# Optimization experiments

Hardware: AMD Instinct MI355X
Metric: run time of the kernel (lower is better)

Reference implementation:

```python
import jax, jax.numpy as jnp
import numpy as np
from itertools import product

DIM = 384
HEADS = 8
DIM_HEAD = 64
INNER = HEADS * DIM_HEAD  # 512
KS = 3                    # kernel_size (attention window)
PAD = KS // 2
W_WIN = KS * KS           # 9
SCALE = DIM_HEAD ** -0.5


def setup_inputs() -> dict:
    key = jax.random.key(0)
    k1, k2, k3, k4, k5 = jax.random.split(key, 5)
    B, H, W = 4, 56, 56
    x = jax.random.normal(k1, (B, DIM, H, W), dtype=jnp.float32)
    # 1x1 conv weights stored as (out_ch, in_ch)
    Wq = jax.random.normal(k2, (INNER, DIM), dtype=jnp.float32) * (DIM ** -0.5)
    Wkv = jax.random.normal(k3, (2 * INNER, DIM), dtype=jnp.float32) * (DIM ** -0.5)
    Wo = jax.random.normal(k4, (DIM, INNER), dtype=jnp.float32) * (INNER ** -0.5)
    bo = jax.random.normal(k5, (DIM,), dtype=jnp.float32) * 0.01
    return {"x": x, "Wq": Wq, "Wkv": Wkv, "Wo": Wo, "bo": bo}


def _conv1x1(x, w):
    # x: (B,Cin,H,W), w: (Cout,Cin) -> (B,Cout,H,W)
    return jnp.einsum('bchw,oc->bohw', x, w)


def reference(x, Wq, Wkv, Wo, bo):
    B, C, H, W = x.shape
    q = _conv1x1(x, Wq)                       # (B, INNER, H, W)
    kv = _conv1x1(x, Wkv)                     # (B, 2*INNER, H, W)
    k, v = jnp.split(kv, 2, axis=1)
    # split channels heads-major, matching torch reshape (B, heads, dh, H, W)
    q = q.reshape(B, HEADS, DIM_HEAD, H, W)
    k = k.reshape(B, HEADS, DIM_HEAD, H, W)
    v = v.reshape(B, HEADS, DIM_HEAD, H, W)
    # zero-pad spatial dims (matches F.unfold zero padding: padded taps get logit 0)
    k_pad = jnp.pad(k, ((0, 0), (0, 0), (0, 0), (PAD, PAD), (PAD, PAD)))
    v_pad = jnp.pad(v, ((0, 0), (0, 0), (0, 0), (PAD, PAD), (PAD, PAD)))
    offsets = list(product(range(KS), range(KS)))  # row-major = unfold order
    # dots: (B, heads, H, W, w)
    dots = jnp.stack([
        jnp.einsum('bhdxy,bhdxy->bhxy', q, k_pad[:, :, :, i:i + H, j:j + W])
        for (i, j) in offsets
    ], axis=-1) * SCALE
    attn = jax.nn.softmax(dots, axis=-1)      # softmax over the 9-tap window
    # weighted sum of shifted v: (B, heads, dh, H, W)
    out = sum(
        attn[:, :, None, :, :, w_idx] * v_pad[:, :, :, i:i + H, j:j + W]
        for w_idx, (i, j) in enumerate(offsets)
    )
    out = out.reshape(B, INNER, H, W)
    return _conv1x1(out, Wo) + bo[None, :, None, None]
```

## Files before the change

### kernel.cpp

```cpp
#include <hip/hip_runtime.h>


#define HW 3136
#define WIMG 56
#define QKV_CH 1536
#define SCALE 0.125f
#define SLEN 200

typedef __bf16 bf16x8_t __attribute__((ext_vector_type(8)));
typedef float f32x4_t __attribute__((ext_vector_type(4)));

__device__ __forceinline__ float bf2f(unsigned short u) {
    return __uint_as_float(((unsigned int)u) << 16);
}
__device__ __forceinline__ unsigned short f2bf(float f) {
    unsigned int u = __float_as_uint(f);
    u += 0x7FFFu + ((u >> 16) & 1u);
    return (unsigned short)(u >> 16);
}

__global__ __launch_bounds__(256) void cvt_w(
    const float* __restrict__ Wq, const float* __restrict__ Wkv,
    const float* __restrict__ Wo,
    unsigned short* __restrict__ wT, unsigned short* __restrict__ wT3)
{
    const int i = blockIdx.x * 256 + threadIdx.x;
    if (i < 73728) {
        const int g = i & 3;
        const int idx3 = i >> 2;
        const int o128 = idx3 & 127;
        const int rest = idx3 >> 7;
        const int kb = rest % 12, oblk = rest / 12;
        const int o = oblk * 128 + o128;
        const int k0 = kb * 32 + g * 8;
        const float* src = (o < 512) ? (Wq + (size_t)o * 384 + k0)
                                     : (Wkv + (size_t)(o - 512) * 384 + k0);
        const float4 v0 = *reinterpret_cast<const float4*>(src);
        const float4 v1 = *reinterpret_cast<const float4*>(src + 4);
        uint4 u;
        u.x = (unsigned int)f2bf(v0.x) | ((unsigned int)f2bf(v0.y) << 16);
        u.y = (unsigned int)f2bf(v0.z) | ((unsigned int)f2bf(v0.w) << 16);
        u.z = (unsigned int)f2bf(v1.x) | ((unsigned int)f2bf(v1.y) << 16);
        u.w = (unsigned int)f2bf(v1.z) | ((unsigned int)f2bf(v1.w) << 16);
        reinterpret_cast<uint4*>(wT)[i] = u;
    } else {
        const int j = i - 73728;
        const int g = j & 3;
        const int idx3 = j >> 2;
        const int o128 = idx3 & 127;
        const int rest = idx3 >> 7;
        const int kb = rest % 16, oblk = rest / 16;
        const int o = oblk * 128 + o128;
        const float* src = Wo + (size_t)o * 512 + kb * 32 + g * 8;
        const float4 v0 = *reinterpret_cast<const float4*>(src);
        const float4 v1 = *reinterpret_cast<const float4*>(src + 4);
        uint4 u;
        u.x = (unsigned int)f2bf(v0.x) | ((unsigned int)f2bf(v0.y) << 16);
        u.y = (unsigned int)f2bf(v0.z) | ((unsigned int)f2bf(v0.w) << 16);
        u.z = (unsigned int)f2bf(v1.x) | ((unsigned int)f2bf(v1.y) << 16);
        u.w = (unsigned int)f2bf(v1.z) | ((unsigned int)f2bf(v1.w) << 16);
        reinterpret_cast<uint4*>(wT3)[j] = u;
    }
}

__global__ __launch_bounds__(256) void cvtT_x(
    const float* __restrict__ x, unsigned short* __restrict__ xT)
{
    __shared__ unsigned short Tl[64 * 36];
    const int sblk = blockIdx.x, kblk = blockIdx.y, b = blockIdx.z;
    const int t = threadIdx.x;

    if (sblk == 49) {
        unsigned short* dst = xT + (((size_t)b * 25 + 24) * 12 + kblk) * 4096 + 2048;
        *reinterpret_cast<uint4*>(dst + t * 8) = (uint4){0, 0, 0, 0};
        return;
    }

    const float* xp = x + ((size_t)b * 384 + (size_t)kblk * 32) * HW + sblk * 64;
    const int c = t >> 3;
#pragma unroll
    for (int i = 0; i < 2; i++) {
        const int sc = (t & 7) + 8 * i;
        const float4 v = *reinterpret_cast<const float4*>(xp + (size_t)c * HW + sc * 4);
        const int s4 = sc * 4;
        Tl[(s4 + 0) * 36 + c] = f2bf(v.x);
        Tl[(s4 + 1) * 36 + c] = f2bf(v.y);
        Tl[(s4 + 2) * 36 + c] = f2bf(v.z);
        Tl[(s4 + 3) * 36 + c] = f2bf(v.w);
    }
    __syncthreads();

    const int row = t >> 2, gran = t & 3;
    const uint2 lo = *reinterpret_cast<const uint2*>(&Tl[row * 36 + gran * 8]);
    const uint2 hi = *reinterpret_cast<const uint2*>(&Tl[row * 36 + gran * 8 + 4]);
    uint4 o; o.x = lo.x; o.y = lo.y; o.z = hi.x; o.w = hi.y;
    unsigned short* dst = xT + (((size_t)b * 25 + (sblk >> 1)) * 12 + kblk) * 4096
                        + (sblk & 1) * 2048;
    *reinterpret_cast<uint4*>(dst + t * 8) = o;
}

__global__ __launch_bounds__(256) void gemm1(
    const unsigned short* __restrict__ xT,
    const unsigned short* __restrict__ wT,
    unsigned short* __restrict__ qkv)
{
    __shared__ __align__(16) unsigned short A_lds[128 * 32];
    __shared__ __align__(16) unsigned short B_lds[128 * 32];

    const int sblk = blockIdx.x;
    const int oblk = blockIdx.y;
    const int b  = blockIdx.z;
    const int t  = threadIdx.x;
    const int lane = t & 63, w = t >> 6;
    const int quad = lane >> 4, mrow = lane & 15;
    const int wm = w >> 1, wn = w & 1;

    const unsigned short* wsrc = wT + ((size_t)oblk * 12) * 4096;
    const unsigned short* xsrc = xT + (((size_t)b * 25 + sblk) * 12) * 4096;

    f32x4_t acc[4][4];
#pragma unroll
    for (int m = 0; m < 4; m++)
#pragma unroll
        for (int n = 0; n < 4; n++) acc[m][n] = (f32x4_t){0.f, 0.f, 0.f, 0.f};

    for (int kb = 0; kb < 12; kb++) {
        const uint4 a0 = *reinterpret_cast<const uint4*>(wsrc + (size_t)kb * 4096 + t * 8);
        const uint4 a1 = *reinterpret_cast<const uint4*>(wsrc + (size_t)kb * 4096 + 2048 + t * 8);
        const uint4 b0 = *reinterpret_cast<const uint4*>(xsrc + (size_t)kb * 4096 + t * 8);
        const uint4 b1 = *reinterpret_cast<const uint4*>(xsrc + (size_t)kb * 4096 + 2048 + t * 8);

        __syncthreads();
        *reinterpret_cast<uint4*>(A_lds + t * 8) = a0;
        *reinterpret_cast<uint4*>(A_lds + 2048 + t * 8) = a1;
        *reinterpret_cast<uint4*>(B_lds + t * 8) = b0;
        *reinterpret_cast<uint4*>(B_lds + 2048 + t * 8) = b1;
        __syncthreads();

        bf16x8_t af[4], bf[4];
#pragma unroll
        for (int m = 0; m < 4; m++)
            af[m] = *reinterpret_cast<const bf16x8_t*>(&A_lds[(wm * 64 + m * 16 + mrow) * 32 + quad * 8]);
#pragma unroll
        for (int n = 0; n < 4; n++)
            bf[n] = *reinterpret_cast<const bf16x8_t*>(&B_lds[(wn * 64 + n * 16 + mrow) * 32 + quad * 8]);
#pragma unroll
        for (int m = 0; m < 4; m++)
#pragma unroll
            for (int n = 0; n < 4; n++)
                acc[m][n] = __builtin_amdgcn_mfma_f32_16x16x32_bf16(af[m], bf[n], acc[m][n], 0, 0, 0);
    }

    const int o0 = oblk * 128 + wm * 64;
    const int s0 = sblk * 128 + wn * 64;
    unsigned short* outb = qkv + (size_t)b * QKV_CH * HW;
#pragma unroll
    for (int m = 0; m < 4; m++)
#pragma unroll
        for (int n = 0; n < 4; n++) {
            const int ss = s0 + n * 16 + mrow;
            if (ss < HW) {
#pragma unroll
                for (int r = 0; r < 4; r++) {
                    const int oo = o0 + m * 16 + quad * 4 + r;
                    outb[(size_t)oo * HW + ss] = f2bf(acc[m][n][r]);
                }
            }
        }
}

__global__ __launch_bounds__(256) void natt2(
    const unsigned short* __restrict__ qkv,
    unsigned short* __restrict__ aoT)
{
    __shared__ __align__(16) unsigned short smem[2 * 64 * SLEN];
    unsigned short* Kl = smem;
    unsigned short* Vl = smem + 64 * SLEN;
    float* dred = reinterpret_cast<float*>(smem);

    const int t = threadIdx.x, lane = t & 63, w = t >> 6;
    const int sblk = blockIdx.x;
    const int s0 = sblk * 64;
    const int s  = s0 + lane;
    const int h  = blockIdx.y, b = blockIdx.z;
    const int y  = s / WIMG, xx = s % WIMG;

    const size_t hbase = (size_t)b * QKV_CH * HW + (size_t)(h * 64) * HW;
    const unsigned short* kg = qkv + hbase + (size_t)512 * HW;
    const unsigned short* vg = qkv + hbase + (size_t)1024 * HW;

#pragma unroll
    for (int i = 0; i < 6; i++) {
        const int f = i * 256 + t;
        const int d = f / 24, j = f % 24;
        int g = s0 - 64 + j * 8;
        g = min(max(g, 0), HW - 8);
        const uint4 k4 = *reinterpret_cast<const uint4*>(kg + (size_t)d * HW + g);
        const uint4 v4 = *reinterpret_cast<const uint4*>(vg + (size_t)d * HW + g);
        *reinterpret_cast<uint4*>(&Kl[d * SLEN + j * 8]) = k4;
        *reinterpret_cast<uint4*>(&Vl[d * SLEN + j * 8]) = v4;
    }

    int   off9[9];
    float msk[9];
#pragma unroll
    for (int ty = 0; ty < 3; ty++)
#pragma unroll
        for (int tx = 0; tx < 3; tx++) {
            const int tap = ty * 3 + tx;
            const int ny = y + ty - 1, nx = xx + tx - 1;
            const bool v = (ny >= 0) && (ny < WIMG) && (nx >= 0) && (nx < WIMG);
            off9[tap] = v ? ((ty - 1) * WIMG + (tx - 1)) : 0;
            msk[tap]  = v ? 1.f : 0.f;
        }

    __syncthreads();

    const unsigned short* qp = qkv + hbase + s;
    float dots[9];
#pragma unroll
    for (int tp = 0; tp < 9; tp++) dots[tp] = 0.f;
#pragma unroll 4
    for (int dd = 0; dd < 16; dd++) {
        const int d = w * 16 + dd;
        const float qv = bf2f(qp[(size_t)d * HW]);
        const int bi = d * SLEN + lane + 64;
#pragma unroll
        for (int tp = 0; tp < 9; tp++)
            dots[tp] += qv * bf2f(Kl[bi + off9[tp]]);
    }

    __syncthreads();
#pragma unroll
    for (int tp = 0; tp < 9; tp++) dred[(tp * 4 + w) * 64 + lane] = dots[tp];
    __syncthreads();

    float mx = -1e30f, dt[9];
#pragma unroll
    for (int tp = 0; tp < 9; tp++) {
        const float sum = dred[(tp * 4 + 0) * 64 + lane] + dred[(tp * 4 + 1) * 64 + lane] +
                          dred[(tp * 4 + 2) * 64 + lane] + dred[(tp * 4 + 3) * 64 + lane];
        dt[tp] = msk[tp] * (sum * SCALE);
        mx = fmaxf(mx, dt[tp]);
    }
    float se = 0.f, w9[9];
#pragma unroll
    for (int tp = 0; tp < 9; tp++) { w9[tp] = __expf(dt[tp] - mx); se += w9[tp]; }
    const float inv = 1.f / se;
#pragma unroll
    for (int tp = 0; tp < 9; tp++) w9[tp] *= inv * msk[tp];

    __align__(16) unsigned short ov[16];
#pragma unroll 4
    for (int dd = 0; dd < 16; dd++) {
        const int d = w * 16 + dd;
        const int bi = d * SLEN + lane + 64;
        float o = 0.f;
#pragma unroll
        for (int tp = 0; tp < 9; tp++)
            o += w9[tp] * bf2f(Vl[bi + off9[tp]]);
        ov[dd] = f2bf(o);
    }
    unsigned short* dst = aoT + (((size_t)(b * 49 + sblk)) * 16 + (h * 2 + (w >> 1))) * 2048
                        + lane * 32 + (w & 1) * 16;
    *reinterpret_cast<uint4*>(dst)     = *reinterpret_cast<const uint4*>(ov);
    *reinterpret_cast<uint4*>(dst + 8) = *reinterpret_cast<const uint4*>(ov + 8);
}

__global__ __launch_bounds__(256) void gemm3(
    const unsigned short* __restrict__ aoT,
    const unsigned short* __restrict__ wT3,
    const float* __restrict__ bias,
    float* __restrict__ out)
{
    __shared__ __align__(16) unsigned short A_lds[128 * 32];
    __shared__ __align__(16) unsigned short B_lds[64 * 32];

    const int sblk = blockIdx.x;
    const int oblk = blockIdx.y;
    const int b  = blockIdx.z;
    const int t  = threadIdx.x;
    const int lane = t & 63, w = t >> 6;
    const int quad = lane >> 4, mrow = lane & 15;
    const int wm = w >> 1, wn = w & 1;

    const unsigned short* asrc = wT3 + (size_t)oblk * 16 * 4096;
    const unsigned short* bsrc = aoT + ((size_t)(b * 49 + sblk)) * 16 * 2048;

    f32x4_t acc[4][2];
#pragma unroll
    for (int m = 0; m < 4; m++)
#pragma unroll
        for (int n = 0; n < 2; n++) acc[m][n] = (f32x4_t){0.f, 0.f, 0.f, 0.f};

    for (int kb = 0; kb < 16; kb++) {
        const uint4 a0 = *reinterpret_cast<const uint4*>(asrc + (size_t)kb * 4096 + t * 8);
        const uint4 a1 = *reinterpret_cast<const uint4*>(asrc + (size_t)kb * 4096 + 2048 + t * 8);
        const uint4 b0 = *reinterpret_cast<const uint4*>(bsrc + (size_t)kb * 2048 + t * 8);

        __syncthreads();
        *reinterpret_cast<uint4*>(A_lds + t * 8) = a0;
        *reinterpret_cast<uint4*>(A_lds + 2048 + t * 8) = a1;
        *reinterpret_cast<uint4*>(B_lds + t * 8) = b0;
        __syncthreads();

        bf16x8_t af[4], bf[2];
#pragma unroll
        for (int m = 0; m < 4; m++)
            af[m] = *reinterpret_cast<const bf16x8_t*>(&A_lds[(wm * 64 + m * 16 + mrow) * 32 + quad * 8]);
#pragma unroll
        for (int n = 0; n < 2; n++)
            bf[n] = *reinterpret_cast<const bf16x8_t*>(&B_lds[(wn * 32 + n * 16 + mrow) * 32 + quad * 8]);
#pragma unroll
        for (int m = 0; m < 4; m++)
#pragma unroll
            for (int n = 0; n < 2; n++)
                acc[m][n] = __builtin_amdgcn_mfma_f32_16x16x32_bf16(af[m], bf[n], acc[m][n], 0, 0, 0);
    }

    const int o0 = oblk * 128 + wm * 64;
    const int s0 = sblk * 64 + wn * 32;
    float* outb = out + (size_t)b * 384 * HW;
#pragma unroll
    for (int m = 0; m < 4; m++)
#pragma unroll
        for (int n = 0; n < 2; n++) {
            const int ss = s0 + n * 16 + mrow;
#pragma unroll
            for (int r = 0; r < 4; r++) {
                const int oo = o0 + m * 16 + quad * 4 + r;
                outb[(size_t)oo * HW + ss] = acc[m][n][r] + bias[oo];
            }
        }
}

extern "C" void kernel_launch(void* const* d_in, const int* in_sizes, int n_in,
                              void* d_out, int out_size, void* d_ws, size_t ws_size,
                              hipStream_t stream) {
    const float* x   = (const float*)d_in[0];
    const float* Wq  = (const float*)d_in[1];
    const float* Wkv = (const float*)d_in[2];
    const float* Wo  = (const float*)d_in[3];
    const float* bo  = (const float*)d_in[4];
    float* out = (float*)d_out;

    unsigned short* xT   = (unsigned short*)d_ws;
    unsigned short* wT   = xT + (size_t)4915200;
    unsigned short* wT3  = wT + (size_t)589824;
    unsigned short* qkvb = wT3 + (size_t)196608;
    unsigned short* aoT  = qkvb + (size_t)4 * QKV_CH * HW;

    cvt_w<<<dim3(384), 256, 0, stream>>>(Wq, Wkv, Wo, wT, wT3);
    cvtT_x<<<dim3(50, 12, 4), 256, 0, stream>>>(x, xT);

    gemm1<<<dim3(25, 12, 4), 256, 0, stream>>>(xT, wT, qkvb);
    natt2<<<dim3(49, 8, 4), 256, 0, stream>>>(qkvb, aoT);
    gemm3<<<dim3(49, 3, 4), 256, 0, stream>>>(aoT, wT3, bo, out);
}
```

Measured before the change: 144.8 us.

## Double-buffer GEMM LDS tiles with direct global-to-LDS async loads

Both projection GEMMs now load tiles straight from global memory into LDS with global_load_lds, skipping the trip through registers. The LDS buffers are doubled so the next k-block's tile is fetched while MFMAs run on the current one, leaving one barrier per iteration instead of two. This is meant to hide global load latency and cut register pressure, at the cost of twice the LDS per block. Correctness relies on the barrier also waiting for the async LDS writes to finish.

After: 148.9 us. +2.8%, slower.

```diff
diff --git a/kernel.cpp b/kernel.cpp
--- a/kernel.cpp
+++ b/kernel.cpp
@@ -17,6 +17,13 @@
     unsigned int u = __float_as_uint(f);
     u += 0x7FFFu + ((u >> 16) & 1u);
     return (unsigned short)(u >> 16);
+}
+
+__device__ __forceinline__ void gll16(const unsigned short* g, unsigned short* l) {
+    __builtin_amdgcn_global_load_lds(
+        (const __attribute__((address_space(1))) unsigned int*)g,
+        (__attribute__((address_space(3))) unsigned int*)l,
+        16, 0, 0);
 }
 
 __global__ __launch_bounds__(256) void cvt_w(
@@ -104,8 +111,8 @@
     const unsigned short* __restrict__ wT,
     unsigned short* __restrict__ qkv)
 {
-    __shared__ __align__(16) unsigned short A_lds[128 * 32];
-    __shared__ __align__(16) unsigned short B_lds[128 * 32];
+    __shared__ __align__(16) unsigned short A_lds[2][128 * 32];
+    __shared__ __align__(16) unsigned short B_lds[2][128 * 32];
 
     const int sblk = blockIdx.x;
     const int oblk = blockIdx.y;
@@ -124,31 +131,39 @@
 #pragma unroll
         for (int n = 0; n < 4; n++) acc[m][n] = (f32x4_t){0.f, 0.f, 0.f, 0.f};
 
+    gll16(wsrc + t * 8,        &A_lds[0][t * 8]);
+    gll16(wsrc + 2048 + t * 8, &A_lds[0][2048 + t * 8]);
+    gll16(xsrc + t * 8,        &B_lds[0][t * 8]);
+    gll16(xsrc + 2048 + t * 8, &B_lds[0][2048 + t * 8]);
+    __syncthreads();
+
+    int cur = 0;
     for (int kb = 0; kb < 12; kb++) {
-        const uint4 a0 = *reinterpret_cast<const uint4*>(wsrc + (size_t)kb * 4096 + t * 8);
-        const uint4 a1 = *reinterpret_cast<const uint4*>(wsrc + (size_t)kb * 4096 + 2048 + t * 8);
-        const uint4 b0 = *reinterpret_cast<const uint4*>(xsrc + (size_t)kb * 4096 + t * 8);
-        const uint4 b1 = *reinterpret_cast<const uint4*>(xsrc + (size_t)kb * 4096 + 2048 + t * 8);
+        if (kb + 1 < 12) {
+            const unsigned short* as = wsrc + (size_t)(kb + 1) * 4096;
+            const unsigned short* bs = xsrc + (size_t)(kb + 1) * 4096;
+            const int nxt = cur ^ 1;
+            gll16(as + t * 8,        &A_lds[nxt][t * 8]);
+            gll16(as + 2048 + t * 8, &A_lds[nxt][2048 + t * 8]);
+            gll16(bs + t * 8,        &B_lds[nxt][t * 8]);
+            gll16(bs + 2048 + t * 8, &B_lds[nxt][2048 + t * 8]);
+        }
+
+        bf16x8_t af[4], bfr[4];
+#pragma unroll
+        for (int m = 0; m < 4; m++)
+            af[m] = *reinterpret_cast<const bf16x8_t*>(&A_lds[cur][(wm * 64 + m * 16 + mrow) * 32 + quad * 8]);
+#pragma unroll
+        for (int n = 0; n < 4; n++)
+            bfr[n] = *reinterpret_cast<const bf16x8_t*>(&B_lds[cur][(wn * 64 + n * 16 + mrow) * 32 + quad * 8]);
+#pragma unroll
+        for (int m = 0; m < 4; m++)
+#pragma unroll
+            for (int n = 0; n < 4; n++)
+                acc[m][n] = __builtin_amdgcn_mfma_f32_16x16x32_bf16(af[m], bfr[n], acc[m][n], 0, 0, 0);
 
         __syncthreads();
-        *reinterpret_cast<uint4*>(A_lds + t * 8) = a0;
-        *reinterpret_cast<uint4*>(A_lds + 2048 + t * 8) = a1;
-        *reinterpret_cast<uint4*>(B_lds + t * 8) = b0;
-        *reinterpret_cast<uint4*>(B_lds + 2048 + t * 8) = b1;
-        __syncthreads();
-
-        bf16x8_t af[4], bf[4];
-#pragma unroll
-        for (int m = 0; m < 4; m++)
-            af[m] = *reinterpret_cast<const bf16x8_t*>(&A_lds[(wm * 64 + m * 16 + mrow) * 32 + quad * 8]);
-#pragma unroll
-        for (int n = 0; n < 4; n++)
-            bf[n] = *reinterpret_cast<const bf16x8_t*>(&B_lds[(wn * 64 + n * 16 + mrow) * 32 + quad * 8]);
-#pragma unroll
-        for (int m = 0; m < 4; m++)
-#pragma unroll
-            for (int n = 0; n < 4; n++)
-                acc[m][n] = __builtin_amdgcn_mfma_f32_16x16x32_bf16(af[m], bf[n], acc[m][n], 0, 0, 0);
+        cur ^= 1;
     }
 
     const int o0 = oblk * 128 + wm * 64;
@@ -273,8 +288,8 @@
     const float* __restrict__ bias,
     float* __restrict__ out)
 {
-    __shared__ __align__(16) unsigned short A_lds[128 * 32];
-    __shared__ __align__(16) unsigned short B_lds[64 * 32];
+    __shared__ __align__(16) unsigned short A_lds[2][128 * 32];
+    __shared__ __align__(16) unsigned short B_lds[2][64 * 32];
 
     const int sblk = blockIdx.x;
     const int oblk = blockIdx.y;
@@ -293,29 +308,37 @@
 #pragma unroll
         for (int n = 0; n < 2; n++) acc[m][n] = (f32x4_t){0.f, 0.f, 0.f, 0.f};
 
+    gll16(asrc + t * 8,        &A_lds[0][t * 8]);
+    gll16(asrc + 2048 + t * 8, &A_lds[0][2048 + t * 8]);
+    gll16(bsrc + t * 8,        &B_lds[0][t * 8]);
+    __syncthreads();
+
+    int cur = 0;
     for (int kb = 0; kb < 16; kb++) {
-        const uint4 a0 = *reinterpret_cast<const uint4*>(asrc + (size_t)kb * 4096 + t * 8);
-        const uint4 a1 = *reinterpret_cast<const uint4*>(asrc + (size_t)kb * 4096 + 2048 + t * 8);
-        const uint4 b0 = *reinterpret_cast<const uint4*>(bsrc + (size_t)kb * 2048 + t * 8);
+        if (kb + 1 < 16) {
+            const unsigned short* as = asrc + (size_t)(kb + 1) * 4096;
+            const unsigned short* bs = bsrc + (size_t)(kb + 1) * 2048;
+            const int nxt = cur ^ 1;
+            gll16(as + t * 8,        &A_lds[nxt][t * 8]);
+            gll16(as + 2048 + t * 8, &A_lds[nxt][2048 + t * 8]);
+            gll16(bs + t * 8,        &B_lds[nxt][t * 8]);
+        }
+
+        bf16x8_t af[4], bfr[2];
+#pragma unroll
+        for (int m = 0; m < 4; m++)
+            af[m] = *reinterpret_cast<const bf16x8_t*>(&A_lds[cur][(wm * 64 + m * 16 + mrow) * 32 + quad * 8]);
+#pragma unroll
+        for (int n = 0; n < 2; n++)
+            bfr[n] = *reinterpret_cast<const bf16x8_t*>(&B_lds[cur][(wn * 32 + n * 16 + mrow) * 32 + quad * 8]);
+#pragma unroll
+        for (int m = 0; m < 4; m++)
+#pragma unroll
+            for (int n = 0; n < 2; n++)
+                acc[m][n] = __builtin_amdgcn_mfma_f32_16x16x32_bf16(af[m], bfr[n], acc[m][n], 0, 0, 0);
 
         __syncthreads();
-        *reinterpret_cast<uint4*>(A_lds + t * 8) = a0;
-        *reinterpret_cast<uint4*>(A_lds + 2048 + t * 8) = a1;
-        *reinterpret_cast<uint4*>(B_lds + t * 8) = b0;
-        __syncthreads();
-
-        bf16x8_t af[4], bf[2];
-#pragma unroll
-        for (int m = 0; m < 4; m++)
-            af[m] = *reinterpret_cast<const bf16x8_t*>(&A_lds[(wm * 64 + m * 16 + mrow) * 32 + quad * 8]);
-#pragma unroll
-        for (int n = 0; n < 2; n++)
-            bf[n] = *reinterpret_cast<const bf16x8_t*>(&B_lds[(wn * 32 + n * 16 + mrow) * 32 + quad * 8]);
-#pragma unroll
-        for (int m = 0; m < 4; m++)
-#pragma unroll
-            for (int n = 0; n < 2; n++)
-                acc[m][n] = __builtin_amdgcn_mfma_f32_16x16x32_bf16(af[m], bf[n], acc[m][n], 0, 0, 0);
+        cur ^= 1;
     }
 
     const int o0 = oblk * 128 + wm * 64;
```

## Store QKV position-major per head so attention reads vectorized channel rows

Applied to the files above, without the earlier changes.

The QKV projection output changes from channel-major (channel × spatial) to a per-head, position-major layout ([q/k/v][b][head][pos][64]). The GEMM epilogue can then write four packed bf16 values per store instead of scattered scalar stores. The attention kernel stages 180 K/V rows with a padded stride into LDS, loads q as two 16-byte vectors, and reads K/V taps as 8-wide vectors rather than scalar reads per channel. The padded LDS stride may still cause bank conflicts, and the larger staging buffer raises shared-memory use per block.

Result: no change. 145.7 us (+0.6%).

```diff
diff --git a/kernel.cpp b/kernel.cpp
--- a/kernel.cpp
+++ b/kernel.cpp
@@ -5,10 +5,13 @@
 #define WIMG 56
 #define QKV_CH 1536
 #define SCALE 0.125f
-#define SLEN 200
+#define KSTR 72
+#define NROWS 180
+#define QKV_T 6422528
 
 typedef __bf16 bf16x8_t __attribute__((ext_vector_type(8)));
 typedef float f32x4_t __attribute__((ext_vector_type(4)));
+typedef unsigned short ushort8 __attribute__((ext_vector_type(8)));
 
 __device__ __forceinline__ float bf2f(unsigned short u) {
     return __uint_as_float(((unsigned int)u) << 16);
@@ -102,7 +105,7 @@
 __global__ __launch_bounds__(256) void gemm1(
     const unsigned short* __restrict__ xT,
     const unsigned short* __restrict__ wT,
-    unsigned short* __restrict__ qkv)
+    unsigned short* __restrict__ qkvT)
 {
     __shared__ __align__(16) unsigned short A_lds[128 * 32];
     __shared__ __align__(16) unsigned short B_lds[128 * 32];
@@ -151,31 +154,34 @@
                 acc[m][n] = __builtin_amdgcn_mfma_f32_16x16x32_bf16(af[m], bf[n], acc[m][n], 0, 0, 0);
     }
 
-    const int o0 = oblk * 128 + wm * 64;
+    const int which = oblk >> 2;
+    const int hq = (oblk & 3) * 2 + wm;
     const int s0 = sblk * 128 + wn * 64;
-    unsigned short* outb = qkv + (size_t)b * QKV_CH * HW;
-#pragma unroll
-    for (int m = 0; m < 4; m++)
+    unsigned short* outb = qkvT + (size_t)which * QKV_T
+                         + ((size_t)(b * 8 + hq) * HW) * 64;
+#pragma unroll
+    for (int m = 0; m < 4; m++) {
+        const int d0 = m * 16 + quad * 4;
 #pragma unroll
         for (int n = 0; n < 4; n++) {
             const int ss = s0 + n * 16 + mrow;
             if (ss < HW) {
-#pragma unroll
-                for (int r = 0; r < 4; r++) {
-                    const int oo = o0 + m * 16 + quad * 4 + r;
-                    outb[(size_t)oo * HW + ss] = f2bf(acc[m][n][r]);
-                }
+                uint2 u;
+                u.x = (unsigned int)f2bf(acc[m][n][0]) | ((unsigned int)f2bf(acc[m][n][1]) << 16);
+                u.y = (unsigned int)f2bf(acc[m][n][2]) | ((unsigned int)f2bf(acc[m][n][3]) << 16);
+                *reinterpret_cast<uint2*>(outb + (size_t)ss * 64 + d0) = u;
             }
         }
+    }
 }
 
 __global__ __launch_bounds__(256) void natt2(
-    const unsigned short* __restrict__ qkv,
+    const unsigned short* __restrict__ qkvT,
     unsigned short* __restrict__ aoT)
 {
-    __shared__ __align__(16) unsigned short smem[2 * 64 * SLEN];
+    __shared__ __align__(16) unsigned short smem[2 * NROWS * KSTR];
     unsigned short* Kl = smem;
-    unsigned short* Vl = smem + 64 * SLEN;
+    unsigned short* Vl = smem + NROWS * KSTR;
     float* dred = reinterpret_cast<float*>(smem);
 
     const int t = threadIdx.x, lane = t & 63, w = t >> 6;
@@ -185,23 +191,25 @@
     const int h  = blockIdx.y, b = blockIdx.z;
     const int y  = s / WIMG, xx = s % WIMG;
 
-    const size_t hbase = (size_t)b * QKV_CH * HW + (size_t)(h * 64) * HW;
-    const unsigned short* kg = qkv + hbase + (size_t)512 * HW;
-    const unsigned short* vg = qkv + hbase + (size_t)1024 * HW;
+    const unsigned short* qg = qkvT + ((size_t)(b * 8 + h) * HW) * 64;
+    const unsigned short* kg = qg + (size_t)QKV_T;
+    const unsigned short* vg = qg + (size_t)(2 * QKV_T);
 
 #pragma unroll
     for (int i = 0; i < 6; i++) {
         const int f = i * 256 + t;
-        const int d = f / 24, j = f % 24;
-        int g = s0 - 64 + j * 8;
-        g = min(max(g, 0), HW - 8);
-        const uint4 k4 = *reinterpret_cast<const uint4*>(kg + (size_t)d * HW + g);
-        const uint4 v4 = *reinterpret_cast<const uint4*>(vg + (size_t)d * HW + g);
-        *reinterpret_cast<uint4*>(&Kl[d * SLEN + j * 8]) = k4;
-        *reinterpret_cast<uint4*>(&Vl[d * SLEN + j * 8]) = v4;
-    }
-
-    int   off9[9];
+        if (f < NROWS * 8) {
+            const int row = f >> 3, c8 = f & 7;
+            int srow = s0 - 59 + row;
+            srow = min(max(srow, 0), HW - 1);
+            const uint4 k4 = *reinterpret_cast<const uint4*>(kg + (size_t)srow * 64 + c8 * 8);
+            const uint4 v4 = *reinterpret_cast<const uint4*>(vg + (size_t)srow * 64 + c8 * 8);
+            *reinterpret_cast<uint4*>(&Kl[row * KSTR + c8 * 8]) = k4;
+            *reinterpret_cast<uint4*>(&Vl[row * KSTR + c8 * 8]) = v4;
+        }
+    }
+
+    int   roff[9];
     float msk[9];
 #pragma unroll
     for (int ty = 0; ty < 3; ty++)
@@ -210,24 +218,40 @@
             const int tap = ty * 3 + tx;
             const int ny = y + ty - 1, nx = xx + tx - 1;
             const bool v = (ny >= 0) && (ny < WIMG) && (nx >= 0) && (nx < WIMG);
-            off9[tap] = v ? ((ty - 1) * WIMG + (tx - 1)) : 0;
+            roff[tap] = (v ? ((ty - 1) * WIMG + (tx - 1)) : 0) * KSTR;
             msk[tap]  = v ? 1.f : 0.f;
         }
 
+    float qv[16];
+    {
+        const uint4 q0 = *reinterpret_cast<const uint4*>(qg + (size_t)s * 64 + w * 16);
+        const uint4 q1 = *reinterpret_cast<const uint4*>(qg + (size_t)s * 64 + w * 16 + 8);
+        qv[0] = bf2f((unsigned short)(q0.x & 0xffff)); qv[1] = bf2f((unsigned short)(q0.x >> 16));
+        qv[2] = bf2f((unsigned short)(q0.y & 0xffff)); qv[3] = bf2f((unsigned short)(q0.y >> 16));
+        qv[4] = bf2f((unsigned short)(q0.z & 0xffff)); qv[5] = bf2f((unsigned short)(q0.z >> 16));
+        qv[6] = bf2f((unsigned short)(q0.w & 0xffff)); qv[7] = bf2f((unsigned short)(q0.w >> 16));
+        qv[8]  = bf2f((unsigned short)(q1.x & 0xffff)); qv[9]  = bf2f((unsigned short)(q1.x >> 16));
+        qv[10] = bf2f((unsigned short)(q1.y & 0xffff)); qv[11] = bf2f((unsigned short)(q1.y >> 16));
+        qv[12] = bf2f((unsigned short)(q1.z & 0xffff)); qv[13] = bf2f((unsigned short)(q1.z >> 16));
+        qv[14] = bf2f((unsigned short)(q1.w & 0xffff)); qv[15] = bf2f((unsigned short)(q1.w >> 16));
+    }
+
     __syncthreads();
 
-    const unsigned short* qp = qkv + hbase + s;
+    const int rbase = (59 + lane) * KSTR + w * 16;
+
     float dots[9];
 #pragma unroll
     for (int tp = 0; tp < 9; tp++) dots[tp] = 0.f;
-#pragma unroll 4
-    for (int dd = 0; dd < 16; dd++) {
-        const int d = w * 16 + dd;
-        const float qv = bf2f(qp[(size_t)d * HW]);
-        const int bi = d * SLEN + lane + 64;
-#pragma unroll
-        for (int tp = 0; tp < 9; tp++)
-            dots[tp] += qv * bf2f(Kl[bi + off9[tp]]);
+#pragma unroll
+    for (int hh = 0; hh < 2; hh++) {
+#pragma unroll
+        for (int tp = 0; tp < 9; tp++) {
+            const ushort8 kk = *reinterpret_cast<const ushort8*>(&Kl[rbase + roff[tp] + hh * 8]);
+#pragma unroll
+            for (int j = 0; j < 8; j++)
+                dots[tp] += qv[hh * 8 + j] * bf2f(kk[j]);
+        }
     }
 
     __syncthreads();
@@ -250,17 +274,26 @@
 #pragma unroll
     for (int tp = 0; tp < 9; tp++) w9[tp] *= inv * msk[tp];
 
+    float o[16];
+#pragma unroll
+    for (int dd = 0; dd < 16; dd++) o[dd] = 0.f;
+#pragma unroll
+    for (int hh = 0; hh < 2; hh++) {
+        ushort8 vfr[9];
+#pragma unroll
+        for (int tp = 0; tp < 9; tp++)
+            vfr[tp] = *reinterpret_cast<const ushort8*>(&Vl[rbase + roff[tp] + hh * 8]);
+#pragma unroll
+        for (int j = 0; j < 8; j++)
+#pragma unroll
+            for (int tp = 0; tp < 9; tp++)
+                o[hh * 8 + j] += w9[tp] * bf2f(vfr[tp][j]);
+    }
+
     __align__(16) unsigned short ov[16];
-#pragma unroll 4
-    for (int dd = 0; dd < 16; dd++) {
-        const int d = w * 16 + dd;
-        const int bi = d * SLEN + lane + 64;
-        float o = 0.f;
-#pragma unroll
-        for (int tp = 0; tp < 9; tp++)
-            o += w9[tp] * bf2f(Vl[bi + off9[tp]]);
-        ov[dd] = f2bf(o);
-    }
+#pragma unroll
+    for (int dd = 0; dd < 16; dd++) ov[dd] = f2bf(o[dd]);
+
     unsigned short* dst = aoT + (((size_t)(b * 49 + sblk)) * 16 + (h * 2 + (w >> 1))) * 2048
                         + lane * 32 + (w & 1) * 16;
     *reinterpret_cast<uint4*>(dst)     = *reinterpret_cast<const uint4*>(ov);
@@ -347,13 +380,13 @@
     unsigned short* xT   = (unsigned short*)d_ws;
     unsigned short* wT   = xT + (size_t)4915200;
     unsigned short* wT3  = wT + (size_t)589824;
-    unsigned short* qkvb = wT3 + (size_t)196608;
-    unsigned short* aoT  = qkvb + (size_t)4 * QKV_CH * HW;
+    unsigned short* qkvT = wT3 + (size_t)196608;
+    unsigned short* aoT  = qkvT + (size_t)(3 * QKV_T);
 
     cvt_w<<<dim3(384), 256, 0, stream>>>(Wq, Wkv, Wo, wT, wT3);
     cvtT_x<<<dim3(50, 12, 4), 256, 0, stream>>>(x, xT);
 
-    gemm1<<<dim3(25, 12, 4), 256, 0, stream>>>(xT, wT, qkvb);
-    natt2<<<dim3(49, 8, 4), 256, 0, stream>>>(qkvb, aoT);
+    gemm1<<<dim3(25, 12, 4), 256, 0, stream>>>(xT, wT, qkvT);
+    natt2<<<dim3(49, 8, 4), 256, 0, stream>>>(qkvT, aoT);
     gemm3<<<dim3(49, 3, 4), 256, 0, stream>>>(aoT, wT3, bo, out);
 }
```
